# Optimization experiments

Measured on AMD Instinct MI355X. Metric: run time of the kernel, lower is better.

## Reference

```python
import jax, jax.numpy as jnp
import numpy as np

L, H, D, DH = 4, 16, 1024, 64   # n_layers, n_heads, d_model, head_dim
VOCAB = 32000
B, S = 2, 2048


def layer_norm(X):
    # Faithful to source: divides by variance (not std), no epsilon.
    mu = jnp.mean(X, axis=2, keepdims=True)
    var = jnp.mean((X - mu) ** 2, axis=2, keepdims=True)
    return (X - mu) / var


def setup_inputs() -> dict:
    key = jax.random.key(0)
    ks = jax.random.split(key, 12)
    s = 0.02
    X = jax.random.normal(ks[0], (B, S, D), dtype=jnp.float32)
    Wq = jax.random.normal(ks[1], (L, H, D, DH), dtype=jnp.float32) * s
    Wk = jax.random.normal(ks[2], (L, H, D, DH), dtype=jnp.float32) * s
    Wv = jax.random.normal(ks[3], (L, H, D, DH), dtype=jnp.float32) * s
    bq = jax.random.normal(ks[4], (L, H, DH), dtype=jnp.float32) * s
    bk = jax.random.normal(ks[5], (L, H, DH), dtype=jnp.float32) * s
    bv = jax.random.normal(ks[6], (L, H, DH), dtype=jnp.float32) * s
    Wffn = jax.random.normal(ks[7], (L, D, D), dtype=jnp.float32) * s
    bffn = jax.random.normal(ks[8], (L, D), dtype=jnp.float32) * s
    Wout = jax.random.normal(ks[9], (D, VOCAB), dtype=jnp.float32) * s
    bout = jax.random.normal(ks[10], (VOCAB,), dtype=jnp.float32) * s
    return {"X": X, "Wq": Wq, "Wk": Wk, "Wv": Wv, "bq": bq, "bk": bk,
            "bv": bv, "Wffn": Wffn, "bffn": bffn, "Wout": Wout, "bout": bout}


def reference(X, Wq, Wk, Wv, bq, bk, bv, Wffn, bffn, Wout, bout):
    sd = jnp.sqrt(jnp.float32(DH))
    for l in range(L):
        # All heads batched: [h, b, s, dh]
        Q = jnp.einsum('bsd,hde->hbse', X, Wq[l]) + bq[l][:, None, None, :]
        K = jnp.einsum('bsd,hde->hbse', X, Wk[l]) + bk[l][:, None, None, :]
        V = jnp.einsum('bsd,hde->hbse', X, Wv[l]) + bv[l][:, None, None, :]
        QK = jnp.einsum('hbse,hbte->hbst', Q, K) / sd
        # Faithful bug: softmax over full row, THEN tril mask (no renorm).
        A = jnp.tril(jax.nn.softmax(QK, axis=-1))
        Z = jnp.einsum('hbst,hbte->hbse', A, V)          # [h,b,s,dh]
        Z = jnp.transpose(Z, (1, 2, 0, 3)).reshape(X.shape[0], X.shape[1], D)
        X = layer_norm(X + Z)                            # note: W_o unused in source
        F = jax.nn.relu(X @ Wffn[l] + bffn[l])
        X = layer_norm(X + F)
    logits = X @ Wout + bout
    return jax.nn.softmax(logits, axis=2)[:, -1, :]
```

## Files before the change

### kernel.cpp

```cpp
#include <hip/hip_runtime.h>
#include <hip/hip_bf16.h>

#define NL 4
#define NH 16
#define DM 1024
#define DHD 64
#define NV 32000
#define NB 2
#define NS 2048
#define NM (NB * NS)

typedef __attribute__((ext_vector_type(8))) short v8s;
typedef __attribute__((ext_vector_type(4))) float v4f;

#define MFMA(a, b, c) __builtin_amdgcn_mfma_f32_16x16x32_bf16(a, b, c, 0, 0, 0)

__device__ __forceinline__ short f2bf(float x) {
    __hip_bfloat16 h = __float2bfloat16(x);
    return *reinterpret_cast<short*>(&h);
}
__device__ __forceinline__ float wave_sum(float v) {
    v += __shfl_xor(v, 32); v += __shfl_xor(v, 16); v += __shfl_xor(v, 8);
    v += __shfl_xor(v, 4);  v += __shfl_xor(v, 2);  v += __shfl_xor(v, 1);
    return v;
}
__device__ __forceinline__ float wave_max(float v) {
    v = fmaxf(v, __shfl_xor(v, 32)); v = fmaxf(v, __shfl_xor(v, 16));
    v = fmaxf(v, __shfl_xor(v, 8));  v = fmaxf(v, __shfl_xor(v, 4));
    v = fmaxf(v, __shfl_xor(v, 2));  v = fmaxf(v, __shfl_xor(v, 1));
    return v;
}

__global__ __launch_bounds__(256) void wqkv_transpose(
    const float* __restrict__ Wq, const float* __restrict__ Wk,
    const float* __restrict__ Wv, __hip_bfloat16* __restrict__ WT)
{
    __shared__ float T[64][68];
    const int t = threadIdx.x;
    const int k0 = blockIdx.x * 64;
    const int y = blockIdx.y;
    const int which = y >> 6, lh = y & 63;
    const float* W = (which == 0 ? Wq : which == 1 ? Wk : Wv)
                     + ((size_t)lh * DM + k0) * DHD;
#pragma unroll
    for (int i = 0; i < 4; ++i) {
        const int f = t + i * 256;
        const int kr = f >> 4, c = (f & 15) * 4;
        float4 w4 = *(const float4*)&W[(size_t)kr * DHD + c];
        T[kr][c + 0] = w4.x; T[kr][c + 1] = w4.y;
        T[kr][c + 2] = w4.z; T[kr][c + 3] = w4.w;
    }
    __syncthreads();
#pragma unroll
    for (int i = 0; i < 2; ++i) {
        const int f = t + i * 256;
        const int n = f >> 3, c = (f & 7) * 8;
        short tmp[8];
#pragma unroll
        for (int j = 0; j < 8; ++j) tmp[j] = f2bf(T[c + j][n]);
        *(float4*)&WT[(((size_t)y) * 64 + n) * DM + k0 + c] = *(float4*)tmp;
    }
}

__global__ __launch_bounds__(256) void wffn_transpose(
    const float* __restrict__ Wffn, __hip_bfloat16* __restrict__ WT)
{
    __shared__ float T[64][68];
    const int t = threadIdx.x;
    const int k0 = blockIdx.x * 64, n0 = blockIdx.y * 64, l = blockIdx.z;
    const float* W = Wffn + ((size_t)l * DM + k0) * DM + n0;
#pragma unroll
    for (int i = 0; i < 4; ++i) {
        const int f = t + i * 256;
        const int kr = f >> 4, c = (f & 15) * 4;
        float4 w4 = *(const float4*)&W[(size_t)kr * DM + c];
        T[kr][c + 0] = w4.x; T[kr][c + 1] = w4.y;
        T[kr][c + 2] = w4.z; T[kr][c + 3] = w4.w;
    }
    __syncthreads();
#pragma unroll
    for (int i = 0; i < 2; ++i) {
        const int f = t + i * 256;
        const int n = f >> 3, c = (f & 7) * 8;
        short tmp[8];
#pragma unroll
        for (int j = 0; j < 8; ++j) tmp[j] = f2bf(T[c + j][n]);
        *(float4*)&WT[((size_t)l * DM + n0 + n) * DM + k0 + c] = *(float4*)tmp;
    }
}

__global__ __launch_bounds__(256) void convert_x0(
    const float* __restrict__ X, __hip_bfloat16* __restrict__ Xh)
{
    const size_t i = ((size_t)blockIdx.x * 256 + threadIdx.x) * 4;
    float4 x = *(const float4*)&X[i];
    union { short s[4]; float2 f2; } hb;
    hb.s[0] = f2bf(x.x); hb.s[1] = f2bf(x.y); hb.s[2] = f2bf(x.z); hb.s[3] = f2bf(x.w);
    *(float2*)&Xh[i] = hb.f2;
}

__global__ __launch_bounds__(256, 2) void qkv_gemm(
    const __hip_bfloat16* __restrict__ Xh, const __hip_bfloat16* __restrict__ WT,
    const float* __restrict__ bq, const float* __restrict__ bk,
    const float* __restrict__ bv,
    __hip_bfloat16* __restrict__ Q, __hip_bfloat16* __restrict__ K,
    __hip_bfloat16* __restrict__ Vt, int layer)
{
    __shared__ short As[128 * 72];
    __shared__ short Bs[192 * 72];
    __shared__ short Vst[64 * 136];
    const int t = threadIdx.x;
    const int wave = t >> 6, lane = t & 63, l15 = lane & 15, quad = lane >> 4;
    const int wm = wave >> 1, wn = wave & 1;
    const int id = blockIdx.y * 32 + blockIdx.x;
    const int x8 = id & 7, j = id >> 3;
    const int m0 = ((x8 & 3) * 8 + (j & 7)) * 128;
    const int h = (x8 >> 2) * 8 + (j >> 3);
    const int lh = layer * NH + h;
    const int arow = t >> 3, ac = (t & 7) * 8;

    v4f acc[4][6];
#pragma unroll
    for (int i = 0; i < 4; ++i)
#pragma unroll
        for (int j2 = 0; j2 < 6; ++j2) acc[i][j2] = 0.f;

    float4 ap[4], bp[6];
#pragma unroll
    for (int i = 0; i < 4; ++i)
        ap[i] = *(const float4*)&Xh[(size_t)(m0 + arow + i * 32) * DM + ac];
#pragma unroll
    for (int i = 0; i < 6; ++i) {
        const int row = arow + i * 32;
        const int which = row >> 6, dh = row & 63;
        bp[i] = *(const float4*)&WT[(((size_t)which * 64 + lh) * 64 + dh) * DM + ac];
    }

    for (int k0 = 0; k0 < DM; k0 += 64) {
        __syncthreads();
#pragma unroll
        for (int i = 0; i < 4; ++i) *(float4*)&As[(arow + i * 32) * 72 + ac] = ap[i];
#pragma unroll
        for (int i = 0; i < 6; ++i) *(float4*)&Bs[(arow + i * 32) * 72 + ac] = bp[i];
        __syncthreads();
        if (k0 + 64 < DM) {
            const int kn = k0 + 64;
#pragma unroll
            for (int i = 0; i < 4; ++i)
                ap[i] = *(const float4*)&Xh[(size_t)(m0 + arow + i * 32) * DM + kn + ac];
#pragma unroll
            for (int i = 0; i < 6; ++i) {
                const int row = arow + i * 32;
                const int which = row >> 6, dh = row & 63;
                bp[i] = *(const float4*)&WT[(((size_t)which * 64 + lh) * 64 + dh) * DM + kn + ac];
            }
        }

        v8s af[4][2];
#pragma unroll
        for (int rt = 0; rt < 4; ++rt)
#pragma unroll
            for (int kh = 0; kh < 2; ++kh)
                af[rt][kh] = *(const v8s*)&As[(wm * 64 + rt * 16 + l15) * 72 + kh * 32 + quad * 8];
#pragma unroll
        for (int ct = 0; ct < 6; ++ct) {
            v8s b0 = *(const v8s*)&Bs[(wn * 96 + ct * 16 + l15) * 72 + quad * 8];
            v8s b1 = *(const v8s*)&Bs[(wn * 96 + ct * 16 + l15) * 72 + 32 + quad * 8];
#pragma unroll
            for (int rt = 0; rt < 4; ++rt) {
                acc[rt][ct] = MFMA(af[rt][0], b0, acc[rt][ct]);
                acc[rt][ct] = MFMA(af[rt][1], b1, acc[rt][ct]);
            }
        }
    }

    __syncthreads();
#pragma unroll
    for (int ct = 0; ct < 6; ++ct) {
        const int n = wn * 96 + ct * 16 + l15;
        const int which = n >> 6;
        const int dh = n & 63;
        const float bias = (which == 0 ? bq : which == 1 ? bk : bv)[(size_t)lh * DHD + dh];
#pragma unroll
        for (int rt = 0; rt < 4; ++rt)
#pragma unroll
            for (int r = 0; r < 4; ++r) {
                const int row = wm * 64 + rt * 16 + quad * 4 + r;
                const short val = f2bf(acc[rt][ct][r] + bias);
                if (which == 0)      As[row * 72 + dh] = val;
                else if (which == 1) Bs[row * 72 + dh] = val;
                else                 Vst[dh * 136 + row] = val;
            }
    }
    __syncthreads();
#pragma unroll
    for (int i = 0; i < 4; ++i) {
        const int f = t + i * 256;
        const int row = f >> 3, c = (f & 7) * 8;
        const int m = m0 + row, bb = m >> 11, s = m & (NS - 1);
        const size_t base = ((size_t)(bb * NH + h) * NS + s) * DHD + c;
        *(float4*)&Q[base] = *(const float4*)&As[row * 72 + c];
        *(float4*)&K[base] = *(const float4*)&Bs[row * 72 + c];
    }
    const int bblk = m0 >> 11;
    const int s0 = m0 & (NS - 1);
    const size_t vtb = (size_t)(bblk * NH + h) * DHD * NS;
#pragma unroll
    for (int i = 0; i < 4; ++i) {
        const int f = t + i * 256;
        const int d = f >> 4, c = (f & 15) * 8;
        *(float4*)&Vt[vtb + (size_t)d * NS + s0 + c] = *(const float4*)&Vst[d * 136 + c];
    }
}

__global__ __launch_bounds__(256, 2) void attn_kernel(
    const __hip_bfloat16* __restrict__ Q, const __hip_bfloat16* __restrict__ K,
    const __hip_bfloat16* __restrict__ Vt, float* __restrict__ Z)
{
    __shared__ short SMEM[4 * 64 * 72 + 128 * 72];
    short* Ks0 = SMEM;
    short* Ks1 = SMEM + 4608;
    short* Vs0 = SMEM + 2 * 4608;
    short* Vs1 = SMEM + 3 * 4608;
    short* Ps  = SMEM + 4 * 4608;
    const int t = threadIdx.x;
    const int w = t >> 6, lane = t & 63, l15 = lane & 15, quad = lane >> 4;
    const int bh = blockIdx.x;
    const int y = blockIdx.y;
    const int bi = (y < 8) ? y : (23 - y);
    const int i0 = bi * 128;
    const int b = bh >> 4, h = bh & 15;
    const size_t qkb = (size_t)bh * NS * DHD;
    const size_t vtb = (size_t)bh * DHD * NS;
    const int arow = t >> 3, ac = (t & 7) * 8;

    v8s aq[2][2];
#pragma unroll
    for (int rt = 0; rt < 2; ++rt) {
        const size_t qrow = qkb + (size_t)(i0 + w * 32 + rt * 16 + l15) * DHD + quad * 8;
        aq[rt][0] = *(const v8s*)&Q[qrow];
        aq[rt][1] = *(const v8s*)&Q[qrow + 32];
    }

    v4f o[2][4];
    float lpart[2][4];
#pragma unroll
    for (int rt = 0; rt < 2; ++rt)
#pragma unroll
        for (int i = 0; i < 4; ++i) { o[rt][i] = 0.f; lpart[rt][i] = 0.f; }

    float4 kf[4], vf[4];
#pragma unroll
    for (int jj = 0; jj < 2; ++jj)
#pragma unroll
        for (int i = 0; i < 2; ++i) {
            const int row = arow + i * 32;
            kf[jj * 2 + i] = *(const float4*)&K[qkb + (size_t)(jj * 64 + row) * DHD + ac];
            vf[jj * 2 + i] = *(const float4*)&Vt[vtb + (size_t)row * NS + jj * 64 + ac];
        }

    for (int wi = 0; wi < 16; ++wi) {
        const bool pv = (wi <= bi);
        __syncthreads();
#pragma unroll
        for (int jj = 0; jj < 2; ++jj)
#pragma unroll
            for (int i = 0; i < 2; ++i) {
                const int row = arow + i * 32;
                *(float4*)&(jj ? Ks1 : Ks0)[row * 72 + ac] = kf[jj * 2 + i];
                if (pv) *(float4*)&(jj ? Vs1 : Vs0)[row * 72 + ac] = vf[jj * 2 + i];
            }
        __syncthreads();
        if (wi < 15) {
            const int n0t = (wi + 1) * 2;
            const bool vneed = (wi + 1 <= bi);
#pragma unroll
            for (int jj = 0; jj < 2; ++jj)
#pragma unroll
                for (int i = 0; i < 2; ++i) {
                    const int row = arow + i * 32;
                    kf[jj * 2 + i] = *(const float4*)&K[qkb + (size_t)((n0t + jj) * 64 + row) * DHD + ac];
                    if (vneed)
                        vf[jj * 2 + i] = *(const float4*)&Vt[vtb + (size_t)row * NS + (n0t + jj) * 64 + ac];
                }
        }

#pragma unroll
        for (int ts = 0; ts < 2; ++ts) {
            const short* Ks = ts ? Ks1 : Ks0;
            const short* Vs = ts ? Vs1 : Vs0;

            v4f s[2][4];
#pragma unroll
            for (int ct = 0; ct < 4; ++ct) {
                v8s b0 = *(const v8s*)&Ks[(ct * 16 + l15) * 72 + quad * 8];
                v8s b1 = *(const v8s*)&Ks[(ct * 16 + l15) * 72 + 32 + quad * 8];
#pragma unroll
                for (int rt = 0; rt < 2; ++rt) {
                    v4f a = 0.f;
                    a = MFMA(aq[rt][0], b0, a);
                    a = MFMA(aq[rt][1], b1, a);
                    s[rt][ct] = a;
                }
            }
#pragma unroll
            for (int rt = 0; rt < 2; ++rt) {
#pragma unroll
                for (int ct = 0; ct < 4; ++ct)
#pragma unroll
                    for (int r = 0; r < 4; ++r)
                        s[rt][ct][r] = __expf(s[rt][ct][r] * 0.125f);
#pragma unroll
                for (int r = 0; r < 4; ++r)
                    lpart[rt][r] += s[rt][0][r] + s[rt][1][r] + s[rt][2][r] + s[rt][3][r];
            }

            if (pv) {
                const bool diag = (wi == bi);
#pragma unroll
                for (int rt = 0; rt < 2; ++rt)
#pragma unroll
                    for (int ct = 0; ct < 4; ++ct)
#pragma unroll
                        for (int r = 0; r < 4; ++r) {
                            const int rowl = w * 32 + rt * 16 + quad * 4 + r;
                            const int col = ct * 16 + l15;
                            float pvv = s[rt][ct][r];
                            if (diag && ts * 64 + col > rowl) pvv = 0.f;
                            Ps[rowl * 72 + col] = f2bf(pvv);
                        }
                v8s ap[2][2];
#pragma unroll
                for (int rt = 0; rt < 2; ++rt) {
                    ap[rt][0] = *(const v8s*)&Ps[(w * 32 + rt * 16 + l15) * 72 + quad * 8];
                    ap[rt][1] = *(const v8s*)&Ps[(w * 32 + rt * 16 + l15) * 72 + 32 + quad * 8];
                }
#pragma unroll
                for (int ct = 0; ct < 4; ++ct) {
                    v8s b0 = *(const v8s*)&Vs[(ct * 16 + l15) * 72 + quad * 8];
                    v8s b1 = *(const v8s*)&Vs[(ct * 16 + l15) * 72 + 32 + quad * 8];
#pragma unroll
                    for (int rt = 0; rt < 2; ++rt) {
                        o[rt][ct] = MFMA(ap[rt][0], b0, o[rt][ct]);
                        o[rt][ct] = MFMA(ap[rt][1], b1, o[rt][ct]);
                    }
                }
            }
        }
    }

#pragma unroll
    for (int m = 1; m < 16; m <<= 1)
#pragma unroll
        for (int rt = 0; rt < 2; ++rt)
#pragma unroll
            for (int r = 0; r < 4; ++r)
                lpart[rt][r] += __shfl_xor(lpart[rt][r], m);

    float* Os = (float*)SMEM;
#pragma unroll
    for (int half = 0; half < 2; ++half) {
        __syncthreads();
        if ((w >> 1) == half) {
#pragma unroll
            for (int rt = 0; rt < 2; ++rt)
#pragma unroll
                for (int r = 0; r < 4; ++r) {
                    const float inv = 1.f / lpart[rt][r];
                    const int row = (w & 1) * 32 + rt * 16 + quad * 4 + r;
#pragma unroll
                    for (int ct = 0; ct < 4; ++ct)
                        Os[row * 68 + ct * 16 + l15] = o[rt][ct][r] * inv;
                }
        }
        __syncthreads();
#pragma unroll
        for (int i = 0; i < 4; ++i) {
            const int f = t + i * 256;
            const int row = f >> 4, c4 = (f & 15) * 4;
            float4 v = *(const float4*)&Os[row * 68 + c4];
            *(float4*)&Z[((size_t)b * NS + i0 + half * 64 + row) * DM + h * DHD + c4] = v;
        }
    }
}

__global__ __launch_bounds__(256, 4) void ffn_gemm(
    const __hip_bfloat16* __restrict__ Xh, const __hip_bfloat16* __restrict__ WT,
    const float* __restrict__ bffn, float* __restrict__ R, int layer)
{
    __shared__ short As[64 * 72];
    __shared__ short Bs[128 * 72];
    const int t = threadIdx.x;
    const int wave = t >> 6, lane = t & 63, l15 = lane & 15, quad = lane >> 4;
    const int wm = wave >> 1, wn = wave & 1;
    const int m0 = blockIdx.x * 64, n0 = blockIdx.y * 128;
    const int arow = t >> 3, ac = (t & 7) * 8;

    v4f acc[2][4];
#pragma unroll
    for (int i = 0; i < 2; ++i)
#pragma unroll
        for (int j = 0; j < 4; ++j) acc[i][j] = 0.f;

    float4 ap[2], bp[4];
#pragma unroll
    for (int i = 0; i < 2; ++i)
        ap[i] = *(const float4*)&Xh[(size_t)(m0 + arow + i * 32) * DM + ac];
#pragma unroll
    for (int i = 0; i < 4; ++i)
        bp[i] = *(const float4*)&WT[((size_t)layer * DM + n0 + arow + i * 32) * DM + ac];

    for (int k0 = 0; k0 < DM; k0 += 64) {
        __syncthreads();
#pragma unroll
        for (int i = 0; i < 2; ++i) *(float4*)&As[(arow + i * 32) * 72 + ac] = ap[i];
#pragma unroll
        for (int i = 0; i < 4; ++i) *(float4*)&Bs[(arow + i * 32) * 72 + ac] = bp[i];
        __syncthreads();
        if (k0 + 64 < DM) {
            const int kn = k0 + 64;
#pragma unroll
            for (int i = 0; i < 2; ++i)
                ap[i] = *(const float4*)&Xh[(size_t)(m0 + arow + i * 32) * DM + kn + ac];
#pragma unroll
            for (int i = 0; i < 4; ++i)
                bp[i] = *(const float4*)&WT[((size_t)layer * DM + n0 + arow + i * 32) * DM + kn + ac];
        }

        v8s af[2][2];
#pragma unroll
        for (int rt = 0; rt < 2; ++rt)
#pragma unroll
            for (int kh = 0; kh < 2; ++kh)
                af[rt][kh] = *(const v8s*)&As[(wm * 32 + rt * 16 + l15) * 72 + kh * 32 + quad * 8];
#pragma unroll
        for (int ct = 0; ct < 4; ++ct) {
            v8s b0 = *(const v8s*)&Bs[(wn * 64 + ct * 16 + l15) * 72 + quad * 8];
            v8s b1 = *(const v8s*)&Bs[(wn * 64 + ct * 16 + l15) * 72 + 32 + quad * 8];
#pragma unroll
            for (int rt = 0; rt < 2; ++rt) {
                acc[rt][ct] = MFMA(af[rt][0], b0, acc[rt][ct]);
                acc[rt][ct] = MFMA(af[rt][1], b1, acc[rt][ct]);
            }
        }
    }
#pragma unroll
    for (int ct = 0; ct < 4; ++ct) {
        const int n = n0 + wn * 64 + ct * 16 + l15;
        const float bias = bffn[(size_t)layer * DM + n];
#pragma unroll
        for (int rt = 0; rt < 2; ++rt)
#pragma unroll
            for (int r = 0; r < 4; ++r) {
                const int m = m0 + wm * 32 + rt * 16 + quad * 4 + r;
                R[(size_t)m * DM + n] = fmaxf(acc[rt][ct][r] + bias, 0.f);
            }
    }
}

__global__ __launch_bounds__(256) void add_ln(
    const float* __restrict__ Xin, const float* __restrict__ Rr,
    float* __restrict__ Xout, __hip_bfloat16* __restrict__ Xh)
{
    __shared__ float red[8];
    const int t = threadIdx.x;
    const size_t base = (size_t)blockIdx.x * DM;
    float4 x4 = *(const float4*)&Xin[base + t * 4];
    float4 r4 = *(const float4*)&Rr[base + t * 4];
    float v[4] = {x4.x + r4.x, x4.y + r4.y, x4.z + r4.z, x4.w + r4.w};
    float ssum = wave_sum(v[0] + v[1] + v[2] + v[3]);
    if ((t & 63) == 0) red[t >> 6] = ssum;
    __syncthreads();
    const float mu = (red[0] + red[1] + red[2] + red[3]) * (1.f / DM);
    float sq = 0.f;
#pragma unroll
    for (int i = 0; i < 4; ++i) { const float d = v[i] - mu; sq = fmaf(d, d, sq); }
    sq = wave_sum(sq);
    if ((t & 63) == 0) red[4 + (t >> 6)] = sq;
    __syncthreads();
    const float var = (red[4] + red[5] + red[6] + red[7]) * (1.f / DM);
    const float inv = 1.f / var;
    float4 o = {(v[0] - mu) * inv, (v[1] - mu) * inv, (v[2] - mu) * inv, (v[3] - mu) * inv};
    *(float4*)&Xout[base + t * 4] = o;
    union { short s[4]; float2 f2; } hb;
    hb.s[0] = f2bf(o.x); hb.s[1] = f2bf(o.y); hb.s[2] = f2bf(o.z); hb.s[3] = f2bf(o.w);
    *(float2*)&Xh[base + t * 4] = hb.f2;
}

__global__ __launch_bounds__(256) void last_logits2(
    const float* __restrict__ X, const float* __restrict__ Wout,
    const float* __restrict__ bout, float* __restrict__ logits)
{
    __shared__ float xs[2 * DM];
    const int t = threadIdx.x;
    for (int k = t; k < 2 * DM; k += 256) {
        const int bb = k >> 10, d = k & (DM - 1);
        xs[k] = X[((size_t)bb * NS + NS - 1) * DM + d];
    }
    __syncthreads();
    const int v = blockIdx.x * 256 + t;
    float a0 = bout[v], a1 = a0;
    for (int d = 0; d < DM; ++d) {
        const float w = Wout[(size_t)d * NV + v];
        a0 = fmaf(xs[d], w, a0);
        a1 = fmaf(xs[DM + d], w, a1);
    }
    logits[v] = a0;
    logits[NV + v] = a1;
}

__global__ __launch_bounds__(256) void final_softmax(
    const float* __restrict__ logits, float* __restrict__ out)
{
    __shared__ float red[8];
    const int b = blockIdx.x, t = threadIdx.x;
    const float* lp = logits + b * NV;
    float mx = -1e30f;
    for (int v = t; v < NV; v += 256) mx = fmaxf(mx, lp[v]);
    mx = wave_max(mx);
    if ((t & 63) == 0) red[t >> 6] = mx;
    __syncthreads();
    mx = fmaxf(fmaxf(red[0], red[1]), fmaxf(red[2], red[3]));
    float sum = 0.f;
    for (int v = t; v < NV; v += 256) sum += __expf(lp[v] - mx);
    sum = wave_sum(sum);
    if ((t & 63) == 0) red[4 + (t >> 6)] = sum;
    __syncthreads();
    sum = red[4] + red[5] + red[6] + red[7];
    const float inv = 1.f / sum;
    for (int v = t; v < NV; v += 256) out[b * NV + v] = __expf(lp[v] - mx) * inv;
}

extern "C" void kernel_launch(void* const* d_in, const int* in_sizes, int n_in,
                              void* d_out, int out_size, void* d_ws, size_t ws_size,
                              hipStream_t stream)
{
    (void)in_sizes; (void)n_in; (void)out_size; (void)ws_size;
    const float* X_in = (const float*)d_in[0];
    const float* Wq   = (const float*)d_in[1];
    const float* Wk   = (const float*)d_in[2];
    const float* Wv   = (const float*)d_in[3];
    const float* bq   = (const float*)d_in[4];
    const float* bk   = (const float*)d_in[5];
    const float* bv   = (const float*)d_in[6];
    const float* Wffn = (const float*)d_in[7];
    const float* bffn = (const float*)d_in[8];
    const float* Wout = (const float*)d_in[9];
    const float* bout = (const float*)d_in[10];
    float* out = (float*)d_out;

    const size_t NE = (size_t)NM * DM;
    char* p = (char*)d_ws;
    float* Xb = (float*)p;                    p += NE * 4;
    float* Rb = (float*)p;                    p += NE * 4;
    float* logits = (float*)p;                p += (size_t)NB * NV * 4;
    __hip_bfloat16* Xhi  = (__hip_bfloat16*)p; p += NE * 2;
    __hip_bfloat16* Qb   = (__hip_bfloat16*)p; p += NE * 2;
    __hip_bfloat16* Kb   = (__hip_bfloat16*)p; p += NE * 2;
    __hip_bfloat16* Vtb  = (__hip_bfloat16*)p; p += NE * 2;
    __hip_bfloat16* WqkvT = (__hip_bfloat16*)p; p += (size_t)3 * 64 * 64 * DM * 2;
    __hip_bfloat16* WffnT = (__hip_bfloat16*)p; p += (size_t)NL * DM * DM * 2;

    wqkv_transpose<<<dim3(16, 192), 256, 0, stream>>>(Wq, Wk, Wv, WqkvT);
    wffn_transpose<<<dim3(16, 16, NL), 256, 0, stream>>>(Wffn, WffnT);
    convert_x0<<<NM, 256, 0, stream>>>(X_in, Xhi);

    for (int l = 0; l < NL; ++l) {
        const float* Xcur = (l == 0) ? X_in : Xb;
        qkv_gemm<<<dim3(32, 16), 256, 0, stream>>>(Xhi, WqkvT, bq, bk, bv, Qb, Kb, Vtb, l);
        attn_kernel<<<dim3(32, 16), 256, 0, stream>>>(Qb, Kb, Vtb, Rb);
        add_ln<<<NM, 256, 0, stream>>>(Xcur, Rb, Xb, Xhi);
        ffn_gemm<<<dim3(64, 8), 256, 0, stream>>>(Xhi, WffnT, bffn, Rb, l);
        add_ln<<<NM, 256, 0, stream>>>(Xb, Rb, Xb, Xhi);
    }
    last_logits2<<<NV / 256, 256, 0, stream>>>(Xb, Wout, bout, logits);
    final_softmax<<<NB, 256, 0, stream>>>(logits, out);
}
```

Measured before the change: 1.469 ms.

## Restructure attention to 512 threads, one 16-row tile per wave, 64-key steps

Attention blocks now use 8 waves of 16 query rows each instead of 4 waves of 32 rows. The key loop walks 64-key tiles one at a time with single K/V shared buffers instead of two tiles per iteration. This halves per-wave register state and shared memory to raise occupancy and latency hiding. In exchange there are twice as many barriers per key range and less reuse of each K/V fragment across row tiles.

```diff
diff --git a/kernel.cpp b/kernel.cpp
--- a/kernel.cpp
+++ b/kernel.cpp
@@ -213,16 +213,14 @@
     }
 }
 
-__global__ __launch_bounds__(256, 2) void attn_kernel(
+__global__ __launch_bounds__(512, 4) void attn_kernel(
     const __hip_bfloat16* __restrict__ Q, const __hip_bfloat16* __restrict__ K,
     const __hip_bfloat16* __restrict__ Vt, float* __restrict__ Z)
 {
-    __shared__ short SMEM[4 * 64 * 72 + 128 * 72];
-    short* Ks0 = SMEM;
-    short* Ks1 = SMEM + 4608;
-    short* Vs0 = SMEM + 2 * 4608;
-    short* Vs1 = SMEM + 3 * 4608;
-    short* Ps  = SMEM + 4 * 4608;
+    __shared__ short SMEM[2 * 64 * 72 + 128 * 72];
+    short* Ks = SMEM;
+    short* Vs = SMEM + 64 * 72;
+    short* Ps = SMEM + 2 * 64 * 72;
     const int t = threadIdx.x;
     const int w = t >> 6, lane = t & 63, l15 = lane & 15, quad = lane >> 4;
     const int bh = blockIdx.x;
@@ -233,150 +231,101 @@
     const size_t qkb = (size_t)bh * NS * DHD;
     const size_t vtb = (size_t)bh * DHD * NS;
     const int arow = t >> 3, ac = (t & 7) * 8;
-
-    v8s aq[2][2];
-#pragma unroll
-    for (int rt = 0; rt < 2; ++rt) {
-        const size_t qrow = qkb + (size_t)(i0 + w * 32 + rt * 16 + l15) * DHD + quad * 8;
-        aq[rt][0] = *(const v8s*)&Q[qrow];
-        aq[rt][1] = *(const v8s*)&Q[qrow + 32];
-    }
-
-    v4f o[2][4];
-    float lpart[2][4];
-#pragma unroll
-    for (int rt = 0; rt < 2; ++rt)
-#pragma unroll
-        for (int i = 0; i < 4; ++i) { o[rt][i] = 0.f; lpart[rt][i] = 0.f; }
-
-    float4 kf[4], vf[4];
-#pragma unroll
-    for (int jj = 0; jj < 2; ++jj)
+    const int r0 = w * 16;
+    const int ktd = 2 * bi + 1;
+
+    const size_t qrow = qkb + (size_t)(i0 + r0 + l15) * DHD + quad * 8;
+    const v8s aq0 = *(const v8s*)&Q[qrow];
+    const v8s aq1 = *(const v8s*)&Q[qrow + 32];
+
+    v4f o[4];
+    float lpart[4] = {0.f, 0.f, 0.f, 0.f};
+#pragma unroll
+    for (int i = 0; i < 4; ++i) o[i] = 0.f;
+
+    float4 kf, vf;
+    kf = *(const float4*)&K[qkb + (size_t)arow * DHD + ac];
+    vf = *(const float4*)&Vt[vtb + (size_t)arow * NS + ac];
+
+    for (int kt = 0; kt < 32; ++kt) {
+        const bool pv = (kt <= ktd);
+        __syncthreads();
+        *(float4*)&Ks[arow * 72 + ac] = kf;
+        if (pv) *(float4*)&Vs[arow * 72 + ac] = vf;
+        __syncthreads();
+        if (kt < 31) {
+            const int nt = kt + 1;
+            kf = *(const float4*)&K[qkb + (size_t)(nt * 64 + arow) * DHD + ac];
+            if (nt <= ktd)
+                vf = *(const float4*)&Vt[vtb + (size_t)arow * NS + nt * 64 + ac];
+        }
+
+        v4f s[4];
+#pragma unroll
+        for (int ct = 0; ct < 4; ++ct) {
+            v8s b0 = *(const v8s*)&Ks[(ct * 16 + l15) * 72 + quad * 8];
+            v8s b1 = *(const v8s*)&Ks[(ct * 16 + l15) * 72 + 32 + quad * 8];
+            v4f a = 0.f;
+            a = MFMA(aq0, b0, a);
+            a = MFMA(aq1, b1, a);
+            s[ct] = a;
+        }
+#pragma unroll
+        for (int ct = 0; ct < 4; ++ct)
+#pragma unroll
+            for (int r = 0; r < 4; ++r)
+                s[ct][r] = __expf(s[ct][r] * 0.125f);
+#pragma unroll
+        for (int r = 0; r < 4; ++r)
+            lpart[r] += s[0][r] + s[1][r] + s[2][r] + s[3][r];
+
+        if (pv) {
+            const int dk = kt - 2 * bi;
+#pragma unroll
+            for (int ct = 0; ct < 4; ++ct)
+#pragma unroll
+                for (int r = 0; r < 4; ++r) {
+                    const int rowl = r0 + quad * 4 + r;
+                    const int col = ct * 16 + l15;
+                    float pvv = s[ct][r];
+                    if (dk >= 0 && dk * 64 + col > rowl) pvv = 0.f;
+                    Ps[rowl * 72 + col] = f2bf(pvv);
+                }
+            v8s ap0 = *(const v8s*)&Ps[(r0 + l15) * 72 + quad * 8];
+            v8s ap1 = *(const v8s*)&Ps[(r0 + l15) * 72 + 32 + quad * 8];
+#pragma unroll
+            for (int ct = 0; ct < 4; ++ct) {
+                v8s b0 = *(const v8s*)&Vs[(ct * 16 + l15) * 72 + quad * 8];
+                v8s b1 = *(const v8s*)&Vs[(ct * 16 + l15) * 72 + 32 + quad * 8];
+                o[ct] = MFMA(ap0, b0, o[ct]);
+                o[ct] = MFMA(ap1, b1, o[ct]);
+            }
+        }
+    }
+
+#pragma unroll
+    for (int m = 1; m < 16; m <<= 1)
+#pragma unroll
+        for (int r = 0; r < 4; ++r) lpart[r] += __shfl_xor(lpart[r], m);
+
+    float* Os = (float*)SMEM;
+#pragma unroll
+    for (int half = 0; half < 2; ++half) {
+        __syncthreads();
+        if ((w >> 2) == half) {
+#pragma unroll
+            for (int r = 0; r < 4; ++r) {
+                const float inv = 1.f / lpart[r];
+                const int row = (w & 3) * 16 + quad * 4 + r;
+#pragma unroll
+                for (int ct = 0; ct < 4; ++ct)
+                    Os[row * 68 + ct * 16 + l15] = o[ct][r] * inv;
+            }
+        }
+        __syncthreads();
 #pragma unroll
         for (int i = 0; i < 2; ++i) {
-            const int row = arow + i * 32;
-            kf[jj * 2 + i] = *(const float4*)&K[qkb + (size_t)(jj * 64 + row) * DHD + ac];
-            vf[jj * 2 + i] = *(const float4*)&Vt[vtb + (size_t)row * NS + jj * 64 + ac];
-        }
-
-    for (int wi = 0; wi < 16; ++wi) {
-        const bool pv = (wi <= bi);
-        __syncthreads();
-#pragma unroll
-        for (int jj = 0; jj < 2; ++jj)
-#pragma unroll
-            for (int i = 0; i < 2; ++i) {
-                const int row = arow + i * 32;
-                *(float4*)&(jj ? Ks1 : Ks0)[row * 72 + ac] = kf[jj * 2 + i];
-                if (pv) *(float4*)&(jj ? Vs1 : Vs0)[row * 72 + ac] = vf[jj * 2 + i];
-            }
-        __syncthreads();
-        if (wi < 15) {
-            const int n0t = (wi + 1) * 2;
-            const bool vneed = (wi + 1 <= bi);
-#pragma unroll
-            for (int jj = 0; jj < 2; ++jj)
-#pragma unroll
-                for (int i = 0; i < 2; ++i) {
-                    const int row = arow + i * 32;
-                    kf[jj * 2 + i] = *(const float4*)&K[qkb + (size_t)((n0t + jj) * 64 + row) * DHD + ac];
-                    if (vneed)
-                        vf[jj * 2 + i] = *(const float4*)&Vt[vtb + (size_t)row * NS + (n0t + jj) * 64 + ac];
-                }
-        }
-
-#pragma unroll
-        for (int ts = 0; ts < 2; ++ts) {
-            const short* Ks = ts ? Ks1 : Ks0;
-            const short* Vs = ts ? Vs1 : Vs0;
-
-            v4f s[2][4];
-#pragma unroll
-            for (int ct = 0; ct < 4; ++ct) {
-                v8s b0 = *(const v8s*)&Ks[(ct * 16 + l15) * 72 + quad * 8];
-                v8s b1 = *(const v8s*)&Ks[(ct * 16 + l15) * 72 + 32 + quad * 8];
-#pragma unroll
-                for (int rt = 0; rt < 2; ++rt) {
-                    v4f a = 0.f;
-                    a = MFMA(aq[rt][0], b0, a);
-                    a = MFMA(aq[rt][1], b1, a);
-                    s[rt][ct] = a;
-                }
-            }
-#pragma unroll
-            for (int rt = 0; rt < 2; ++rt) {
-#pragma unroll
-                for (int ct = 0; ct < 4; ++ct)
-#pragma unroll
-                    for (int r = 0; r < 4; ++r)
-                        s[rt][ct][r] = __expf(s[rt][ct][r] * 0.125f);
-#pragma unroll
-                for (int r = 0; r < 4; ++r)
-                    lpart[rt][r] += s[rt][0][r] + s[rt][1][r] + s[rt][2][r] + s[rt][3][r];
-            }
-
-            if (pv) {
-                const bool diag = (wi == bi);
-#pragma unroll
-                for (int rt = 0; rt < 2; ++rt)
-#pragma unroll
-                    for (int ct = 0; ct < 4; ++ct)
-#pragma unroll
-                        for (int r = 0; r < 4; ++r) {
-                            const int rowl = w * 32 + rt * 16 + quad * 4 + r;
-                            const int col = ct * 16 + l15;
-                            float pvv = s[rt][ct][r];
-                            if (diag && ts * 64 + col > rowl) pvv = 0.f;
-                            Ps[rowl * 72 + col] = f2bf(pvv);
-                        }
-                v8s ap[2][2];
-#pragma unroll
-                for (int rt = 0; rt < 2; ++rt) {
-                    ap[rt][0] = *(const v8s*)&Ps[(w * 32 + rt * 16 + l15) * 72 + quad * 8];
-                    ap[rt][1] = *(const v8s*)&Ps[(w * 32 + rt * 16 + l15) * 72 + 32 + quad * 8];
-                }
-#pragma unroll
-                for (int ct = 0; ct < 4; ++ct) {
-                    v8s b0 = *(const v8s*)&Vs[(ct * 16 + l15) * 72 + quad * 8];
-                    v8s b1 = *(const v8s*)&Vs[(ct * 16 + l15) * 72 + 32 + quad * 8];
-#pragma unroll
-                    for (int rt = 0; rt < 2; ++rt) {
-                        o[rt][ct] = MFMA(ap[rt][0], b0, o[rt][ct]);
-                        o[rt][ct] = MFMA(ap[rt][1], b1, o[rt][ct]);
-                    }
-                }
-            }
-        }
-    }
-
-#pragma unroll
-    for (int m = 1; m < 16; m <<= 1)
-#pragma unroll
-        for (int rt = 0; rt < 2; ++rt)
-#pragma unroll
-            for (int r = 0; r < 4; ++r)
-                lpart[rt][r] += __shfl_xor(lpart[rt][r], m);
-
-    float* Os = (float*)SMEM;
-#pragma unroll
-    for (int half = 0; half < 2; ++half) {
-        __syncthreads();
-        if ((w >> 1) == half) {
-#pragma unroll
-            for (int rt = 0; rt < 2; ++rt)
-#pragma unroll
-                for (int r = 0; r < 4; ++r) {
-                    const float inv = 1.f / lpart[rt][r];
-                    const int row = (w & 1) * 32 + rt * 16 + quad * 4 + r;
-#pragma unroll
-                    for (int ct = 0; ct < 4; ++ct)
-                        Os[row * 68 + ct * 16 + l15] = o[rt][ct][r] * inv;
-                }
-        }
-        __syncthreads();
-#pragma unroll
-        for (int i = 0; i < 4; ++i) {
-            const int f = t + i * 256;
+            const int f = t + i * 512;
             const int row = f >> 4, c4 = (f & 15) * 4;
             float4 v = *(const float4*)&Os[row * 68 + c4];
             *(float4*)&Z[((size_t)b * NS + i0 + half * 64 + row) * DM + h * DHD + c4] = v;
@@ -568,7 +517,7 @@
     for (int l = 0; l < NL; ++l) {
         const float* Xcur = (l == 0) ? X_in : Xb;
         qkv_gemm<<<dim3(32, 16), 256, 0, stream>>>(Xhi, WqkvT, bq, bk, bv, Qb, Kb, Vtb, l);
-        attn_kernel<<<dim3(32, 16), 256, 0, stream>>>(Qb, Kb, Vtb, Rb);
+        attn_kernel<<<dim3(32, 16), 512, 0, stream>>>(Qb, Kb, Vtb, Rb);
         add_ln<<<NM, 256, 0, stream>>>(Xcur, Rb, Xb, Xhi);
         ffn_gemm<<<dim3(64, 8), 256, 0, stream>>>(Xhi, WffnT, bffn, Rb, l);
         add_ln<<<NM, 256, 0, stream>>>(Xb, Rb, Xb, Xhi);
```

Result: faster. 1.249 ms (-15.0%).
